# Optimization experiments

Hardware: AMD Instinct MI355X
Metric: run time of the kernel (lower is better)

Reference implementation:

```python
import jax, jax.numpy as jnp
import numpy as np

KP_EXTENT = 1.2  # influence radius of each kernel point (init arg KP_extent)
SHADOW_COORD = 1e6  # shadow point coordinate for padding (as in original KPConv)


def setup_inputs() -> dict:
    key = jax.random.key(0)
    k1, k2, k3, k4, k5, k6 = jax.random.split(key, 6)
    N, Ns, H, K, Cin, Cout = 20000, 20000, 40, 15, 128, 128
    q_pts = jax.random.uniform(k1, (N, 3), dtype=jnp.float32)
    s_pts = jax.random.uniform(k2, (Ns, 3), dtype=jnp.float32)
    neighb_inds = jax.random.randint(k3, (N, H), 0, Ns, dtype=jnp.int32)
    x = jax.random.normal(k4, (Ns, Cin), dtype=jnp.float32)
    # kernel point positions inside the sphere (stand-in for load_kernels output)
    kernel_points = jax.random.normal(k5, (K, 3), dtype=jnp.float32) * 0.5
    kernel_points = kernel_points.at[0].set(0.0)  # fixed='center'
    weights = jax.random.normal(k6, (K, Cin, Cout), dtype=jnp.float32) * (1.0 / np.sqrt(Cin))
    return {"q_pts": q_pts, "s_pts": s_pts, "neighb_inds": neighb_inds,
            "x": x, "kernel_points": kernel_points, "weights": weights}


def reference(q_pts, s_pts, neighb_inds, x, kernel_points, weights):
    # Pad support points with a far-away shadow point and features with a zero row,
    # so out-of-range neighbor index Ns contributes nothing (original KPConv trick).
    s_pad = jnp.concatenate([s_pts, jnp.full((1, s_pts.shape[1]), SHADOW_COORD, s_pts.dtype)], axis=0)
    x_pad = jnp.concatenate([x, jnp.zeros((1, x.shape[1]), x.dtype)], axis=0)

    # Gather neighbor coords, center on query points: [N, H, 3]
    neighbors = s_pad[neighb_inds] - q_pts[:, None, :]

    # Squared distance to every kernel point: [N, H, K]
    diff = neighbors[:, :, None, :] - kernel_points[None, None, :, :]
    sq_dist = jnp.sum(diff * diff, axis=-1)

    # Linear influence weights, aggregation_mode='sum': [N, K, H]
    all_weights = jnp.clip(1.0 - jnp.sqrt(sq_dist) / KP_EXTENT, 0.0, None)
    all_weights = jnp.swapaxes(all_weights, 1, 2)

    # Gather neighbor features: [N, H, Cin]
    neighb_x = x_pad[neighb_inds]

    # Influence-weighted aggregation over neighbors: [N, K, Cin]
    weighted = jnp.einsum('nkh,nhc->nkc', all_weights, neighb_x)

    # Per-kernel-point linear maps, summed over kernel points: [N, Cout]
    out = jnp.einsum('nkc,kcd->nd', weighted, weights)
    return out
```

## Files before the change

### kernel.cpp

```cpp
#include <hip/hip_runtime.h>

#define KP   15
#define HN   40
#define CIN  128
#define COUT 128
#define KDIM (KP*CIN)
#define KP_EXT_INV (1.0f/1.2f)

typedef __bf16 bf16x8 __attribute__((ext_vector_type(8)));
typedef __bf16 bf16x4 __attribute__((ext_vector_type(4)));
typedef float  f32x4  __attribute__((ext_vector_type(4)));

__device__ inline void async_copy16(const void* g, void* lds) {
    __builtin_amdgcn_global_load_lds(
        (const __attribute__((address_space(1))) unsigned int*)g,
        (__attribute__((address_space(3))) unsigned int*)lds, 16, 0, 0);
}
#define LGKM0() __asm__ __volatile__("s_waitcnt lgkmcnt(0)" ::: "memory")

__global__ __launch_bounds__(256)
void kpconv_prep(const float* __restrict__ x, const float* __restrict__ W,
                 __bf16* __restrict__ xb, __bf16* __restrict__ Wt,
                 int nx_elems, int nxB)
{
    __shared__ float sW[32][133];
    const int b = blockIdx.x;
    const int t = threadIdx.x;

    if (b < nxB) {
        const int e0 = (b*256 + t) * 8;
        if (e0 + 8 <= nx_elems) {
            const float4 f0 = *(const float4*)(x + e0);
            const float4 f1 = *(const float4*)(x + e0 + 4);
            bf16x8 v;
            v[0]=(__bf16)f0.x; v[1]=(__bf16)f0.y; v[2]=(__bf16)f0.z; v[3]=(__bf16)f0.w;
            v[4]=(__bf16)f1.x; v[5]=(__bf16)f1.y; v[6]=(__bf16)f1.z; v[7]=(__bf16)f1.w;
            *(bf16x8*)(xb + e0) = v;
        } else {
            for (int e = e0; e < nx_elems; ++e) xb[e] = (__bf16)x[e];
        }
    } else {
        const int kc0 = (b - nxB) * 32;
        #pragma unroll
        for (int i = 0; i < 4; ++i) {
            const int off = t*4 + i*1024;
            const int r = off >> 7, c = off & 127;
            const float4 f = *(const float4*)(W + (size_t)(kc0 + r)*COUT + c);
            sW[r][c+0]=f.x; sW[r][c+1]=f.y; sW[r][c+2]=f.z; sW[r][c+3]=f.w;
        }
        __syncthreads();
        #pragma unroll
        for (int i = 0; i < 2; ++i) {
            const int id = t + i*256;
            const int d  = id >> 2, ch = id & 3;
            bf16x8 v;
            #pragma unroll
            for (int j = 0; j < 8; ++j) v[j] = (__bf16)sW[ch*8 + j][d];
            *(bf16x8*)(Wt + (size_t)d*KDIM + kc0 + ch*8) = v;
        }
    }
}

__global__ __launch_bounds__(64, 4)
void kpconv_aggregate(const float* __restrict__ q_pts,
                      const float* __restrict__ s_pts,
                      const int*   __restrict__ nb,
                      const __bf16* __restrict__ xb,
                      const float* __restrict__ kpts,
                      __bf16* __restrict__ wsA,
                      int N, int Ns)
{
    __shared__ __align__(16) __bf16 sXt[4][128][8];
    __shared__ __align__(16) float4 s_nd[HN];
    __shared__ int                  s_idx[HN];

    const int l = threadIdx.x;
    const int m = l & 15;
    const int q = l >> 4;
    const int n = blockIdx.x;

    if (l < HN) {
        int idx = nb[n*HN + l];
        float dx, dy, dz;
        if (idx >= 0 && idx < Ns) {
            dx = s_pts[idx*3+0] - q_pts[n*3+0];
            dy = s_pts[idx*3+1] - q_pts[n*3+1];
            dz = s_pts[idx*3+2] - q_pts[n*3+2];
        } else { idx = 0; dx = dy = dz = 2.0e6f; }
        s_idx[l] = idx;
        s_nd[l]  = make_float4(dx, dy, dz, dx*dx + dy*dy + dz*dz);
    }
    LGKM0();

    uint4 g[5][2];
    #pragma unroll
    for (int it = 0; it < 5; ++it) {
        const int h0 = (it < 4) ? (it*8 + 2*q) : (32 + 2*q);
        g[it][0] = *(const uint4*)(xb + (size_t)s_idx[h0  ]*CIN + m*8);
        g[it][1] = *(const uint4*)(xb + (size_t)s_idx[h0+1]*CIN + m*8);
    }

    float kx=0.f, ky=0.f, kz=0.f;
    if (m < KP) { kx = kpts[m*3+0]; ky = kpts[m*3+1]; kz = kpts[m*3+2]; }
    const float kk  = kx*kx + ky*ky + kz*kz;
    const float kx2 = -2.f*kx, ky2 = -2.f*ky, kz2 = -2.f*kz;

    bf16x8 wfrag[2];
    #pragma unroll
    for (int ks = 0; ks < 2; ++ks) {
        #pragma unroll
        for (int j = 0; j < 8; ++j) {
            const int h = ks*32 + q*8 + j;
            float w = 0.f;
            if (m < KP && h < HN) {
                const float4 nd = s_nd[h];
                const float d2 = fmaf(nd.x, kx2,
                                 fmaf(nd.y, ky2,
                                 fmaf(nd.z, kz2, nd.w + kk)));
                const float d = __builtin_amdgcn_sqrtf(d2);
                w = fmaxf(fmaf(d, -KP_EXT_INV, 1.0f), 0.f);
            }
            wfrag[ks][j] = (__bf16)w;
        }
    }

    f32x4 acc[8];
    #pragma unroll
    for (int nt = 0; nt < 8; ++nt) acc[nt] = (f32x4){0.f,0.f,0.f,0.f};

    #pragma unroll
    for (int ks = 0; ks < 2; ++ks) {
        const int itBeg = ks ? 4 : 0;
        const int itEnd = ks ? 5 : 4;
        #pragma unroll
        for (int it = itBeg; it < itEnd; ++it) {
            const unsigned av[4] = {g[it][0].x, g[it][0].y, g[it][0].z, g[it][0].w};
            const unsigned bv[4] = {g[it][1].x, g[it][1].y, g[it][1].z, g[it][1].w};
            const int hc = ks ? 0 : it;
            unsigned* plane = (unsigned*)&sXt[hc][0][0];
            #pragma unroll
            for (int j = 0; j < 8; ++j) {
                const unsigned v = __builtin_amdgcn_perm(
                    bv[j>>1], av[j>>1], (j&1) ? 0x07060302u : 0x05040100u);
                const int p = m*8 + (j ^ (m & 7));
                plane[p*4 + q] = v;
            }
        }
        LGKM0();

        #pragma unroll
        for (int nt = 0; nt < 8; ++nt) {
            const int cc = nt*16 + m;
            const int p  = (cc & ~7) | ((cc & 7) ^ ((cc >> 3) & 7));
            bf16x8 xf = *(const bf16x8*)&sXt[q][p][0];
            acc[nt] = __builtin_amdgcn_mfma_f32_16x16x32_bf16(
                          xf, wfrag[ks], acc[nt], 0, 0, 0);
        }
    }

    if (m < KP) {
        #pragma unroll
        for (int nt = 0; nt < 8; ++nt) {
            bf16x4 v;
            #pragma unroll
            for (int r = 0; r < 4; ++r) v[r] = (__bf16)acc[nt][r];
            *(bf16x4*)(wsA + (size_t)n*KDIM + m*CIN + nt*16 + q*4) = v;
        }
    }
}

#define GBM 32
#define GBK 128

__global__ __launch_bounds__(256, 4)
void kpconv_gemm(const __bf16* __restrict__ A,
                 const __bf16* __restrict__ Bt,
                 float* __restrict__ out, int M)
{
    __shared__ __align__(16) __bf16 sA[GBM*GBK];
    __shared__ __align__(16) __bf16 sB[COUT*GBK];

    const int t     = threadIdx.x;
    const int wv    = t >> 6;
    const int l     = t & 63;
    const int mlane = l & 15;
    const int q     = l >> 4;
    const int m0    = blockIdx.x * GBM;

    const int itBeg = blockIdx.y ? 8 : 0;
    const int itEnd = blockIdx.y ? 15 : 8;

    const int rA = t >> 4;
    const int pA = t & 15;

    f32x4 acc[2][2];
    #pragma unroll
    for (int i = 0; i < 2; ++i)
        #pragma unroll
        for (int j = 0; j < 2; ++j) acc[i][j] = (f32x4){0.f,0.f,0.f,0.f};

    for (int it = itBeg; it < itEnd; ++it) {
        const int k0 = it * GBK;
        #pragma unroll
        for (int pass = 0; pass < 2; ++pass) {
            const int r  = rA + pass*16;
            const int ch = pA ^ (r & 15);
            async_copy16(A + (size_t)(m0 + r)*KDIM + k0 + ch*8,
                         (char*)sA + pass*4096 + wv*1024 + l*16);
        }
        #pragma unroll
        for (int pass = 0; pass < 8; ++pass) {
            const int r  = rA + pass*16;
            const int ch = pA ^ (r & 15);
            async_copy16(Bt + (size_t)r*KDIM + k0 + ch*8,
                         (char*)sB + pass*4096 + wv*1024 + l*16);
        }
        __syncthreads();

        #pragma unroll
        for (int ks = 0; ks < 4; ++ks) {
            bf16x8 af[2], bfr[2];
            #pragma unroll
            for (int mt = 0; mt < 2; ++mt) {
                const int row = mt*16 + mlane;
                const int p   = (ks*4 + q) ^ (row & 15);
                af[mt] = *(const bf16x8*)&sA[row*GBK + p*8];
            }
            #pragma unroll
            for (int j = 0; j < 2; ++j) {
                const int row = (wv*2 + j)*16 + mlane;
                const int p   = (ks*4 + q) ^ (row & 15);
                bfr[j] = *(const bf16x8*)&sB[row*GBK + p*8];
            }
            #pragma unroll
            for (int mt = 0; mt < 2; ++mt)
                #pragma unroll
                for (int j = 0; j < 2; ++j)
                    acc[mt][j] = __builtin_amdgcn_mfma_f32_16x16x32_bf16(
                                     af[mt], bfr[j], acc[mt][j], 0, 0, 0);
        }
        __syncthreads();
    }

    #pragma unroll
    for (int mt = 0; mt < 2; ++mt)
        #pragma unroll
        for (int j = 0; j < 2; ++j)
            #pragma unroll
            for (int r = 0; r < 4; ++r)
                atomicAdd(&out[(size_t)(m0 + mt*16 + q*4 + r)*COUT
                               + (wv*2+j)*16 + mlane], acc[mt][j][r]);
}

#define TM 8
#define WSTR (KP*CIN + 4)

__global__ __launch_bounds__(256, 2)
void kpconv_fused(const float* __restrict__ q_pts,
                  const float* __restrict__ s_pts,
                  const int*   __restrict__ nb,
                  const float* __restrict__ x,
                  const float* __restrict__ kpts,
                  const float* __restrict__ W,
                  float* __restrict__ out,
                  int N, int Ns)
{
    __shared__ float s_kp[KP*3];
    __shared__ float s_nd2[HN*3];
    __shared__ int   s_idx2[HN];
    __shared__ float s_w[KP][HN];
    __shared__ float s_wt[TM*WSTR];

    const int t  = threadIdx.x;
    const int n0 = (int)blockIdx.x * TM;
    if (t < KP*3) s_kp[t] = kpts[t];
    const int c = t & (CIN-1);
    const int g = t >> 7;

    for (int mm = 0; mm < TM; ++mm) {
        const int n = n0 + mm;
        if (t < HN) {
            float dx = 1e6f, dy = 1e6f, dz = 1e6f;
            int idx = 0;
            if (n < N) {
                idx = nb[n*HN + t];
                if (idx >= 0 && idx < Ns) {
                    dx = s_pts[idx*3+0] - q_pts[n*3+0];
                    dy = s_pts[idx*3+1] - q_pts[n*3+1];
                    dz = s_pts[idx*3+2] - q_pts[n*3+2];
                } else idx = 0;
            }
            s_idx2[t] = idx;
            s_nd2[t*3+0] = dx; s_nd2[t*3+1] = dy; s_nd2[t*3+2] = dz;
        }
        __syncthreads();
        for (int task = t; task < KP*HN; task += 256) {
            const int k = task / HN;
            const int h = task - k*HN;
            const float dx = s_nd2[h*3+0] - s_kp[k*3+0];
            const float dy = s_nd2[h*3+1] - s_kp[k*3+1];
            const float dz = s_nd2[h*3+2] - s_kp[k*3+2];
            s_w[k][h] = fmaxf(1.0f - sqrtf(dx*dx+dy*dy+dz*dz)*KP_EXT_INV, 0.0f);
        }
        __syncthreads();
        float facc[8];
        #pragma unroll
        for (int j = 0; j < 8; ++j) facc[j] = 0.0f;
        #pragma unroll 8
        for (int h = 0; h < HN; ++h) {
            const float xv = x[s_idx2[h]*CIN + c];
            #pragma unroll
            for (int j = 0; j < 8; ++j) {
                const int k = g + 2*j;
                if (k < KP) facc[j] += s_w[k][h] * xv;
            }
        }
        #pragma unroll
        for (int j = 0; j < 8; ++j) {
            const int k = g + 2*j;
            if (k < KP) s_wt[mm*WSTR + k*CIN + c] = facc[j];
        }
        __syncthreads();
    }

    const int m3 = t >> 5;
    const int d0 = (t & 31) * 4;
    const float* wm = &s_wt[m3*WSTR];
    float ax = 0.f, ay = 0.f, az = 0.f, aw = 0.f;
    #pragma unroll 4
    for (int kc = 0; kc < KP*CIN; ++kc) {
        const float  wvv = wm[kc];
        const float4 wr = *(const float4*)&W[kc*COUT + d0];
        ax += wvv * wr.x; ay += wvv * wr.y; az += wvv * wr.z; aw += wvv * wr.w;
    }
    const int n = n0 + m3;
    if (n < N) {
        float4 o; o.x = ax; o.y = ay; o.z = az; o.w = aw;
        *(float4*)&out[n*COUT + d0] = o;
    }
}

extern "C" void kernel_launch(void* const* d_in, const int* in_sizes, int n_in,
                              void* d_out, int out_size, void* d_ws, size_t ws_size,
                              hipStream_t stream) {
    const float* q_pts = (const float*)d_in[0];
    const float* s_pts = (const float*)d_in[1];
    const int*   nb    = (const int*)  d_in[2];
    const float* x     = (const float*)d_in[3];
    const float* kpts  = (const float*)d_in[4];
    const float* W     = (const float*)d_in[5];
    float* out = (float*)d_out;

    const int N  = in_sizes[0] / 3;
    const int Ns = in_sizes[1] / 3;
    const int nx = in_sizes[3];

    const size_t needA = (size_t)N * KDIM * sizeof(__bf16);
    const size_t needB = (size_t)COUT * KDIM * sizeof(__bf16);
    const size_t needX = (size_t)nx * sizeof(__bf16);

    if (ws_size >= needA + needB + needX && (N % GBM) == 0 && (KDIM % 128) == 0) {
        __bf16* wsA = (__bf16*)d_ws;
        __bf16* wsB = (__bf16*)((char*)d_ws + needA);
        __bf16* wsX = (__bf16*)((char*)d_ws + needA + needB);

        const int nxB = (nx/8 + 255) / 256;
        const int nwB = KDIM / 32;
        hipMemsetAsync(out, 0, (size_t)out_size * sizeof(float), stream);
        hipLaunchKernelGGL(kpconv_prep, dim3(nxB + nwB), dim3(256), 0, stream,
                           x, W, wsX, wsB, nx, nxB);
        hipLaunchKernelGGL(kpconv_aggregate, dim3(N), dim3(64), 0, stream,
                           q_pts, s_pts, nb, wsX, kpts, wsA, N, Ns);
        hipLaunchKernelGGL(kpconv_gemm, dim3(N/GBM, 2), dim3(256), 0, stream,
                           wsA, wsB, out, N);
    } else {
        const int grid = (N + TM - 1) / TM;
        hipLaunchKernelGGL(kpconv_fused, dim3(grid), dim3(256), 0, stream,
                           q_pts, s_pts, nb, x, kpts, W, out, N, Ns);
    }
}
```

Measured before the change: 144.1 us.

## Fuse aggregation and GEMM into one kernel per 32-row tile, drop split-K atomics

Merges the per-point aggregation kernel and the bf16 GEMM into a single kernel. Each 256-thread block first aggregates its 32 query points, with each wave handling 8 points, and writes them to the workspace. It then runs the full-K GEMM on that tile, so the intermediate rows are likely still in L2 when re-read. Dropping split-K removes the memset and the atomicAdd output, replacing them with plain stores, and also removes one launch. In exchange, the grid shrinks to N/32 blocks, the aggregation phase is serialized within each wave, and there is less parallelism than the former two-way split-K.

```diff
diff --git a/kernel.cpp b/kernel.cpp
--- a/kernel.cpp
+++ b/kernel.cpp
@@ -6,6 +6,8 @@
 #define COUT 128
 #define KDIM (KP*CIN)
 #define KP_EXT_INV (1.0f/1.2f)
+#define GBM  32
+#define GBK  128
 
 typedef __bf16 bf16x8 __attribute__((ext_vector_type(8)));
 typedef __bf16 bf16x4 __attribute__((ext_vector_type(4)));
@@ -17,6 +19,7 @@
         (__attribute__((address_space(3))) unsigned int*)lds, 16, 0, 0);
 }
 #define LGKM0() __asm__ __volatile__("s_waitcnt lgkmcnt(0)" ::: "memory")
+#define VM0()   __asm__ __volatile__("s_waitcnt vmcnt(0)"   ::: "memory")
 
 __global__ __launch_bounds__(256)
 void kpconv_prep(const float* __restrict__ x, const float* __restrict__ W,
@@ -61,195 +64,189 @@
     }
 }
 
-__global__ __launch_bounds__(64, 4)
-void kpconv_aggregate(const float* __restrict__ q_pts,
-                      const float* __restrict__ s_pts,
-                      const int*   __restrict__ nb,
-                      const __bf16* __restrict__ xb,
-                      const float* __restrict__ kpts,
-                      __bf16* __restrict__ wsA,
-                      int N, int Ns)
+union SharedU {
+    struct { __bf16 sXt[4][4][128][8];
+             float4 s_nd[4][HN]; int s_idx[4][HN]; } a;
+    struct { __bf16 sA[GBM*GBK]; __bf16 sB[COUT*GBK]; } b;
+};
+
+__global__ __launch_bounds__(256, 3)
+void kpconv_main(const float* __restrict__ q_pts,
+                 const float* __restrict__ s_pts,
+                 const int*   __restrict__ nb,
+                 const __bf16* __restrict__ xb,
+                 const float* __restrict__ kpts,
+                 const __bf16* __restrict__ Wt,
+                 __bf16* __restrict__ wsA,
+                 float* __restrict__ out, int N, int Ns)
 {
-    __shared__ __align__(16) __bf16 sXt[4][128][8];
-    __shared__ __align__(16) float4 s_nd[HN];
-    __shared__ int                  s_idx[HN];
-
-    const int l = threadIdx.x;
-    const int m = l & 15;
-    const int q = l >> 4;
-    const int n = blockIdx.x;
-
-    if (l < HN) {
-        int idx = nb[n*HN + l];
-        float dx, dy, dz;
-        if (idx >= 0 && idx < Ns) {
-            dx = s_pts[idx*3+0] - q_pts[n*3+0];
-            dy = s_pts[idx*3+1] - q_pts[n*3+1];
-            dz = s_pts[idx*3+2] - q_pts[n*3+2];
-        } else { idx = 0; dx = dy = dz = 2.0e6f; }
-        s_idx[l] = idx;
-        s_nd[l]  = make_float4(dx, dy, dz, dx*dx + dy*dy + dz*dz);
-    }
-    LGKM0();
-
-    uint4 g[5][2];
-    #pragma unroll
-    for (int it = 0; it < 5; ++it) {
-        const int h0 = (it < 4) ? (it*8 + 2*q) : (32 + 2*q);
-        g[it][0] = *(const uint4*)(xb + (size_t)s_idx[h0  ]*CIN + m*8);
-        g[it][1] = *(const uint4*)(xb + (size_t)s_idx[h0+1]*CIN + m*8);
-    }
-
-    float kx=0.f, ky=0.f, kz=0.f;
-    if (m < KP) { kx = kpts[m*3+0]; ky = kpts[m*3+1]; kz = kpts[m*3+2]; }
-    const float kk  = kx*kx + ky*ky + kz*kz;
-    const float kx2 = -2.f*kx, ky2 = -2.f*ky, kz2 = -2.f*kz;
-
-    bf16x8 wfrag[2];
-    #pragma unroll
-    for (int ks = 0; ks < 2; ++ks) {
-        #pragma unroll
-        for (int j = 0; j < 8; ++j) {
-            const int h = ks*32 + q*8 + j;
-            float w = 0.f;
-            if (m < KP && h < HN) {
-                const float4 nd = s_nd[h];
-                const float d2 = fmaf(nd.x, kx2,
-                                 fmaf(nd.y, ky2,
-                                 fmaf(nd.z, kz2, nd.w + kk)));
-                const float d = __builtin_amdgcn_sqrtf(d2);
-                w = fmaxf(fmaf(d, -KP_EXT_INV, 1.0f), 0.f);
-            }
-            wfrag[ks][j] = (__bf16)w;
-        }
-    }
-
-    f32x4 acc[8];
-    #pragma unroll
-    for (int nt = 0; nt < 8; ++nt) acc[nt] = (f32x4){0.f,0.f,0.f,0.f};
-
-    #pragma unroll
-    for (int ks = 0; ks < 2; ++ks) {
-        const int itBeg = ks ? 4 : 0;
-        const int itEnd = ks ? 5 : 4;
-        #pragma unroll
-        for (int it = itBeg; it < itEnd; ++it) {
-            const unsigned av[4] = {g[it][0].x, g[it][0].y, g[it][0].z, g[it][0].w};
-            const unsigned bv[4] = {g[it][1].x, g[it][1].y, g[it][1].z, g[it][1].w};
-            const int hc = ks ? 0 : it;
-            unsigned* plane = (unsigned*)&sXt[hc][0][0];
-            #pragma unroll
-            for (int j = 0; j < 8; ++j) {
-                const unsigned v = __builtin_amdgcn_perm(
-                    bv[j>>1], av[j>>1], (j&1) ? 0x07060302u : 0x05040100u);
-                const int p = m*8 + (j ^ (m & 7));
-                plane[p*4 + q] = v;
-            }
-        }
-        LGKM0();
-
-        #pragma unroll
-        for (int nt = 0; nt < 8; ++nt) {
-            const int cc = nt*16 + m;
-            const int p  = (cc & ~7) | ((cc & 7) ^ ((cc >> 3) & 7));
-            bf16x8 xf = *(const bf16x8*)&sXt[q][p][0];
-            acc[nt] = __builtin_amdgcn_mfma_f32_16x16x32_bf16(
-                          xf, wfrag[ks], acc[nt], 0, 0, 0);
-        }
-    }
-
-    if (m < KP) {
-        #pragma unroll
-        for (int nt = 0; nt < 8; ++nt) {
-            bf16x4 v;
-            #pragma unroll
-            for (int r = 0; r < 4; ++r) v[r] = (__bf16)acc[nt][r];
-            *(bf16x4*)(wsA + (size_t)n*KDIM + m*CIN + nt*16 + q*4) = v;
-        }
-    }
-}
-
-#define GBM 32
-#define GBK 128
-
-__global__ __launch_bounds__(256, 4)
-void kpconv_gemm(const __bf16* __restrict__ A,
-                 const __bf16* __restrict__ Bt,
-                 float* __restrict__ out, int M)
-{
-    __shared__ __align__(16) __bf16 sA[GBM*GBK];
-    __shared__ __align__(16) __bf16 sB[COUT*GBK];
-
-    const int t     = threadIdx.x;
-    const int wv    = t >> 6;
-    const int l     = t & 63;
-    const int mlane = l & 15;
-    const int q     = l >> 4;
-    const int m0    = blockIdx.x * GBM;
-
-    const int itBeg = blockIdx.y ? 8 : 0;
-    const int itEnd = blockIdx.y ? 15 : 8;
-
-    const int rA = t >> 4;
-    const int pA = t & 15;
-
-    f32x4 acc[2][2];
-    #pragma unroll
-    for (int i = 0; i < 2; ++i)
-        #pragma unroll
-        for (int j = 0; j < 2; ++j) acc[i][j] = (f32x4){0.f,0.f,0.f,0.f};
-
-    for (int it = itBeg; it < itEnd; ++it) {
-        const int k0 = it * GBK;
-        #pragma unroll
-        for (int pass = 0; pass < 2; ++pass) {
-            const int r  = rA + pass*16;
-            const int ch = pA ^ (r & 15);
-            async_copy16(A + (size_t)(m0 + r)*KDIM + k0 + ch*8,
-                         (char*)sA + pass*4096 + wv*1024 + l*16);
-        }
-        #pragma unroll
-        for (int pass = 0; pass < 8; ++pass) {
-            const int r  = rA + pass*16;
-            const int ch = pA ^ (r & 15);
-            async_copy16(Bt + (size_t)r*KDIM + k0 + ch*8,
-                         (char*)sB + pass*4096 + wv*1024 + l*16);
-        }
-        __syncthreads();
-
-        #pragma unroll
-        for (int ks = 0; ks < 4; ++ks) {
-            bf16x8 af[2], bfr[2];
-            #pragma unroll
-            for (int mt = 0; mt < 2; ++mt) {
-                const int row = mt*16 + mlane;
-                const int p   = (ks*4 + q) ^ (row & 15);
-                af[mt] = *(const bf16x8*)&sA[row*GBK + p*8];
-            }
-            #pragma unroll
-            for (int j = 0; j < 2; ++j) {
-                const int row = (wv*2 + j)*16 + mlane;
-                const int p   = (ks*4 + q) ^ (row & 15);
-                bfr[j] = *(const bf16x8*)&sB[row*GBK + p*8];
-            }
-            #pragma unroll
-            for (int mt = 0; mt < 2; ++mt)
-                #pragma unroll
-                for (int j = 0; j < 2; ++j)
-                    acc[mt][j] = __builtin_amdgcn_mfma_f32_16x16x32_bf16(
-                                     af[mt], bfr[j], acc[mt][j], 0, 0, 0);
-        }
-        __syncthreads();
-    }
-
-    #pragma unroll
-    for (int mt = 0; mt < 2; ++mt)
-        #pragma unroll
-        for (int j = 0; j < 2; ++j)
-            #pragma unroll
-            for (int r = 0; r < 4; ++r)
-                atomicAdd(&out[(size_t)(m0 + mt*16 + q*4 + r)*COUT
-                               + (wv*2+j)*16 + mlane], acc[mt][j][r]);
+    __shared__ SharedU sh;
+
+    const int t  = threadIdx.x;
+    const int wv = t >> 6;
+    const int l  = t & 63;
+    const int m  = l & 15;
+    const int q  = l >> 4;
+    const int m0 = blockIdx.x * GBM;
+
+    {
+        float kx=0.f, ky=0.f, kz=0.f;
+        if (m < KP) { kx = kpts[m*3+0]; ky = kpts[m*3+1]; kz = kpts[m*3+2]; }
+        const float kk  = kx*kx + ky*ky + kz*kz;
+        const float kx2 = -2.f*kx, ky2 = -2.f*ky, kz2 = -2.f*kz;
+
+        for (int pi = 0; pi < 8; ++pi) {
+            const int n = m0 + wv*8 + pi;
+
+            if (l < HN) {
+                int idx = nb[n*HN + l];
+                float dx, dy, dz;
+                if (idx >= 0 && idx < Ns) {
+                    dx = s_pts[idx*3+0] - q_pts[n*3+0];
+                    dy = s_pts[idx*3+1] - q_pts[n*3+1];
+                    dz = s_pts[idx*3+2] - q_pts[n*3+2];
+                } else { idx = 0; dx = dy = dz = 2.0e6f; }
+                sh.a.s_idx[wv][l] = idx;
+                sh.a.s_nd[wv][l]  = make_float4(dx, dy, dz, dx*dx+dy*dy+dz*dz);
+            }
+            LGKM0();
+
+            uint4 g[5][2];
+            #pragma unroll
+            for (int it = 0; it < 5; ++it) {
+                const int h0 = (it < 4) ? (it*8 + 2*q) : (32 + 2*q);
+                g[it][0] = *(const uint4*)(xb + (size_t)sh.a.s_idx[wv][h0  ]*CIN + m*8);
+                g[it][1] = *(const uint4*)(xb + (size_t)sh.a.s_idx[wv][h0+1]*CIN + m*8);
+            }
+
+            bf16x8 wfrag[2];
+            #pragma unroll
+            for (int ks = 0; ks < 2; ++ks) {
+                #pragma unroll
+                for (int j = 0; j < 8; ++j) {
+                    const int h = ks*32 + q*8 + j;
+                    float w = 0.f;
+                    if (m < KP && h < HN) {
+                        const float4 nd = sh.a.s_nd[wv][h];
+                        const float d2 = fmaf(nd.x, kx2,
+                                         fmaf(nd.y, ky2,
+                                         fmaf(nd.z, kz2, nd.w + kk)));
+                        const float d = __builtin_amdgcn_sqrtf(d2);
+                        w = fmaxf(fmaf(d, -KP_EXT_INV, 1.0f), 0.f);
+                    }
+                    wfrag[ks][j] = (__bf16)w;
+                }
+            }
+
+            f32x4 acc[8];
+            #pragma unroll
+            for (int nt = 0; nt < 8; ++nt) acc[nt] = (f32x4){0.f,0.f,0.f,0.f};
+
+            #pragma unroll
+            for (int ks = 0; ks < 2; ++ks) {
+                const int itBeg = ks ? 4 : 0;
+                const int itEnd = ks ? 5 : 4;
+                #pragma unroll
+                for (int it = itBeg; it < itEnd; ++it) {
+                    const unsigned av[4] = {g[it][0].x, g[it][0].y, g[it][0].z, g[it][0].w};
+                    const unsigned bv[4] = {g[it][1].x, g[it][1].y, g[it][1].z, g[it][1].w};
+                    const int hc = ks ? 0 : it;
+                    unsigned* plane = (unsigned*)&sh.a.sXt[wv][hc][0][0];
+                    #pragma unroll
+                    for (int j = 0; j < 8; ++j) {
+                        const unsigned v = __builtin_amdgcn_perm(
+                            bv[j>>1], av[j>>1], (j&1) ? 0x07060302u : 0x05040100u);
+                        const int p = m*8 + (j ^ (m & 7));
+                        plane[p*4 + q] = v;
+                    }
+                }
+                LGKM0();
+                #pragma unroll
+                for (int nt = 0; nt < 8; ++nt) {
+                    const int cc = nt*16 + m;
+                    const int p  = (cc & ~7) | ((cc & 7) ^ ((cc >> 3) & 7));
+                    bf16x8 xf = *(const bf16x8*)&sh.a.sXt[wv][q][p][0];
+                    acc[nt] = __builtin_amdgcn_mfma_f32_16x16x32_bf16(
+                                  xf, wfrag[ks], acc[nt], 0, 0, 0);
+                }
+            }
+
+            if (m < KP) {
+                #pragma unroll
+                for (int nt = 0; nt < 8; ++nt) {
+                    bf16x4 v;
+                    #pragma unroll
+                    for (int r = 0; r < 4; ++r) v[r] = (__bf16)acc[nt][r];
+                    *(bf16x4*)(wsA + (size_t)n*KDIM + m*CIN + nt*16 + q*4) = v;
+                }
+            }
+        }
+    }
+
+    VM0();
+    __syncthreads();
+
+    {
+        const int rA = t >> 4;
+        const int pA = t & 15;
+
+        f32x4 acc[2][2];
+        #pragma unroll
+        for (int i = 0; i < 2; ++i)
+            #pragma unroll
+            for (int j = 0; j < 2; ++j) acc[i][j] = (f32x4){0.f,0.f,0.f,0.f};
+
+        for (int k0 = 0; k0 < KDIM; k0 += GBK) {
+            #pragma unroll
+            for (int pass = 0; pass < 2; ++pass) {
+                const int r  = rA + pass*16;
+                const int ch = pA ^ (r & 15);
+                async_copy16(wsA + (size_t)(m0 + r)*KDIM + k0 + ch*8,
+                             (char*)sh.b.sA + pass*4096 + wv*1024 + l*16);
+            }
+            #pragma unroll
+            for (int pass = 0; pass < 8; ++pass) {
+                const int r  = rA + pass*16;
+                const int ch = pA ^ (r & 15);
+                async_copy16(Wt + (size_t)r*KDIM + k0 + ch*8,
+                             (char*)sh.b.sB + pass*4096 + wv*1024 + l*16);
+            }
+            __syncthreads();
+
+            #pragma unroll
+            for (int ks = 0; ks < 4; ++ks) {
+                bf16x8 af[2], bfr[2];
+                #pragma unroll
+                for (int mt = 0; mt < 2; ++mt) {
+                    const int row = mt*16 + m;
+                    const int p   = (ks*4 + q) ^ (row & 15);
+                    af[mt] = *(const bf16x8*)&sh.b.sA[row*GBK + p*8];
+                }
+                #pragma unroll
+                for (int j = 0; j < 2; ++j) {
+                    const int row = (wv*2 + j)*16 + m;
+                    const int p   = (ks*4 + q) ^ (row & 15);
+                    bfr[j] = *(const bf16x8*)&sh.b.sB[row*GBK + p*8];
+                }
+                #pragma unroll
+                for (int mt = 0; mt < 2; ++mt)
+                    #pragma unroll
+                    for (int j = 0; j < 2; ++j)
+                        acc[mt][j] = __builtin_amdgcn_mfma_f32_16x16x32_bf16(
+                                         af[mt], bfr[j], acc[mt][j], 0, 0, 0);
+            }
+            __syncthreads();
+        }
+
+        #pragma unroll
+        for (int mt = 0; mt < 2; ++mt)
+            #pragma unroll
+            for (int j = 0; j < 2; ++j)
+                #pragma unroll
+                for (int r = 0; r < 4; ++r)
+                    out[(size_t)(m0 + mt*16 + q*4 + r)*COUT
+                        + (wv*2+j)*16 + m] = acc[mt][j][r];
+    }
 }
 
 #define TM 8
@@ -359,20 +356,18 @@
     const size_t needB = (size_t)COUT * KDIM * sizeof(__bf16);
     const size_t needX = (size_t)nx * sizeof(__bf16);
 
-    if (ws_size >= needA + needB + needX && (N % GBM) == 0 && (KDIM % 128) == 0) {
+    if (ws_size >= needA + needB + needX && (N % GBM) == 0 && (nx % 8) == 0
+        && (KDIM % GBK) == 0) {
         __bf16* wsA = (__bf16*)d_ws;
         __bf16* wsB = (__bf16*)((char*)d_ws + needA);
         __bf16* wsX = (__bf16*)((char*)d_ws + needA + needB);
 
         const int nxB = (nx/8 + 255) / 256;
         const int nwB = KDIM / 32;
-        hipMemsetAsync(out, 0, (size_t)out_size * sizeof(float), stream);
         hipLaunchKernelGGL(kpconv_prep, dim3(nxB + nwB), dim3(256), 0, stream,
                            x, W, wsX, wsB, nx, nxB);
-        hipLaunchKernelGGL(kpconv_aggregate, dim3(N), dim3(64), 0, stream,
-                           q_pts, s_pts, nb, wsX, kpts, wsA, N, Ns);
-        hipLaunchKernelGGL(kpconv_gemm, dim3(N/GBM, 2), dim3(256), 0, stream,
-                           wsA, wsB, out, N);
+        hipLaunchKernelGGL(kpconv_main, dim3(N/GBM), dim3(256), 0, stream,
+                           q_pts, s_pts, nb, wsX, kpts, wsB, wsA, out, N, Ns);
     } else {
         const int grid = (N + TM - 1) / TM;
         hipLaunchKernelGGL(kpconv_fused, dim3(grid), dim3(256), 0, stream,
```

Measured after the change: 143.7 us (median of 2 runs). No clear change (-0.3%).
